# Kernel optimization log

Measured on AMD Instinct MI355X. Metric: run time of the kernel, lower is better.

Reference implementation:

```python
import jax, jax.numpy as jnp
import numpy as np

N = 20000       # nodes
E = 320000      # edges (avg in-degree 16)
IN_DIM = 128
HID = 64
HEADS = 4
NUM_GRAPHS = 128
N_CLASSES = 10


def setup_inputs() -> dict:
    key = jax.random.key(0)
    ks = jax.random.split(key, 8)
    h = jax.random.normal(ks[0], (N, IN_DIM), jnp.float32)
    src = jax.random.randint(ks[1], (E,), 0, N)
    dst = jax.random.randint(ks[2], (E,), 0, N)
    graph_ids = jnp.sort(jax.random.randint(ks[3], (N,), 0, NUM_GRAPHS))
    # DotGatConv fc weights (no bias in DGL DotGatConv), classifier Linear w/ bias
    W1 = jax.random.normal(ks[4], (IN_DIM, HID * HEADS), jnp.float32) / np.sqrt(IN_DIM).astype(np.float32)
    W2 = jax.random.normal(ks[5], (HID * HEADS, HID), jnp.float32) / np.sqrt(HID * HEADS).astype(np.float32)
    Wc = jax.random.normal(ks[6], (HID, N_CLASSES), jnp.float32) / np.sqrt(HID).astype(np.float32)
    bc = jnp.zeros((N_CLASSES,), jnp.float32)
    return {"h": h, "src": src, "dst": dst, "graph_ids": graph_ids,
            "W1": W1, "W2": W2, "Wc": Wc, "bc": bc}


def dot_gat(x, src, dst, W, num_heads):
    """DGL DotGatConv: scaled dot-product attention over graph edges."""
    n = x.shape[0]
    d = W.shape[1] // num_heads
    ft = (x @ W).reshape(n, num_heads, d)          # [N,H,D]
    hs = ft[src]                                    # [E,H,D] source feats
    hd = ft[dst]                                    # [E,H,D] dest feats
    e = (hs * hd).sum(-1) / jnp.sqrt(jnp.float32(d))  # [E,H] edge scores
    # edge softmax over incoming edges per destination node (stable)
    m = jax.ops.segment_max(e, dst, num_segments=n)    # [N,H]
    ee = jnp.exp(e - m[dst])                           # [E,H]
    den = jax.ops.segment_sum(ee, dst, num_segments=n)[dst]  # [E,H]
    a = ee / den
    # aggregate attention-weighted source messages at destination
    return jax.ops.segment_sum(hs * a[..., None], dst, num_segments=n)  # [N,H,D]


def reference(h, src, dst, graph_ids, W1, W2, Wc, bc):
    n = h.shape[0]
    x = jax.nn.relu(dot_gat(h, src, dst, W1, HEADS)).reshape(n, -1)   # [N, HID*HEADS]
    x = jax.nn.relu(dot_gat(x, src, dst, W2, 1)).reshape(n, -1)       # [N, HID]
    # AvgPooling: mean of node features per graph
    cnt = jax.ops.segment_sum(jnp.ones((n,), x.dtype), graph_ids, num_segments=NUM_GRAPHS)
    pooled = jax.ops.segment_sum(x, graph_ids, num_segments=NUM_GRAPHS) / jnp.maximum(cnt, 1.0)[:, None]
    return pooled @ Wc + bc                                            # [NUM_GRAPHS, N_CLASSES]
```

## Files before the change

### kernel.cpp

```cpp
#include <hip/hip_runtime.h>
#include <hip/hip_bf16.h>

typedef __attribute__((ext_vector_type(8))) __bf16 bf16x8;
typedef __attribute__((ext_vector_type(4))) float floatx4;

#define N_NODES   20000
#define N_EDGES   320000
#define IN_DIM    128
#define HID       64
#define HEADS     4
#define NUM_GRAPHS 128
#define N_CLASSES 10

__device__ inline float cvt_load(const void* p, int i, int isb) {
    return isb ? __bfloat162float(((const __hip_bfloat16*)p)[i]) : ((const float*)p)[i];
}

__device__ inline unsigned short bf16bits(float v) {
    return __builtin_bit_cast(unsigned short, __float2bfloat16(v));
}

__device__ inline unsigned pack2(float a, float b) {
    return (unsigned)bf16bits(a) | ((unsigned)bf16bits(b) << 16);
}

__device__ inline floatx4 unpack4(uint2 u) {
    floatx4 f;
    f.x = __uint_as_float(u.x << 16);
    f.y = __uint_as_float(u.x & 0xffff0000u);
    f.z = __uint_as_float(u.y << 16);
    f.w = __uint_as_float(u.y & 0xffff0000u);
    return f;
}

__global__ void init_kernel(const unsigned int* hw, int nwords, int* flag,
                            unsigned int* cnt, int n1, unsigned int* gz, int n2) {
    int b = blockIdx.x;
    if (b == 0) {
        __shared__ int s_bad;
        if (threadIdx.x == 0) s_bad = 0;
        __syncthreads();
        int bad = 0;
        for (int i = threadIdx.x; i < nwords; i += 256) {
            float v = __uint_as_float(hw[i]);
            if (!(fabsf(v) <= 1e20f)) bad = 1;
        }
        if (bad) atomicOr(&s_bad, 1);
        __syncthreads();
        if (threadIdx.x == 0) *flag = s_bad;
    } else {
        int i = (b - 1) * 256 + threadIdx.x;
        if (i < n1) cnt[i] = 0u;
        int j = i - n1;
        if (j >= 0 && j < n2) gz[j] = 0u;
    }
}

__global__ void prep_kernel(const void* W1, const void* W2, const void* Wc, const void* bc,
                            unsigned short* W1t, unsigned short* W2t, float* Wcf, float* bcf,
                            const void* h, unsigned short* hb,
                            const int* __restrict__ dst, int* __restrict__ cnt,
                            const int* flag) {
    int b = blockIdx.x;
    const int n1 = IN_DIM * HID * HEADS;
    const int n2 = HID * HEADS * HID;
    const int n3 = HID * N_CLASSES;
    const int n4 = N_CLASSES;
    if (b < 195) {
        int i = b * 256 + threadIdx.x;
        int isb = *flag;
        if (i < n1) {
            int k = i >> 8, n = i & 255;
            W1t[n * 128 + k] = bf16bits(cvt_load(W1, i, isb));
        } else if (i < n1 + n2) {
            int j = i - n1;
            int k = j >> 6, n = j & 63;
            W2t[n * 256 + k] = bf16bits(cvt_load(W2, j, isb));
        } else if (i < n1 + n2 + n3) {
            int j = i - n1 - n2;
            Wcf[j] = cvt_load(Wc, j, isb);
        } else if (i < n1 + n2 + n3 + n4) {
            int j = i - n1 - n2 - n3;
            bcf[j] = cvt_load(bc, j, isb);
        }
    } else if (b < 195 + 640) {
        int isb = *flag;
        if (!isb) {
            int base = (b - 195) * 4096;
            for (int t = 0; t < 16; ++t) {
                int i = base + t * 256 + threadIdx.x;
                if (i < N_NODES * IN_DIM) hb[i] = bf16bits(cvt_load(h, i, 0));
            }
        }
    } else {
        int e = (b - 835) * 256 + threadIdx.x;
        if (e < N_EDGES) atomicAdd(&cnt[dst[e]], 1);
    }
}

__global__ void scan_kernel(const int* __restrict__ cnt, int* __restrict__ off,
                            int* __restrict__ off_work, int n) {
    const int CH = 20;
    __shared__ int wsum[16];
    int tid  = threadIdx.x;
    int lane = tid & 63;
    int w    = tid >> 6;
    int base = tid * CH;
    int local[CH];
    int s = 0;
#pragma unroll
    for (int i = 0; i < CH; ++i) {
        int idx = base + i;
        int v = (idx < n) ? cnt[idx] : 0;
        local[i] = s;
        s += v;
    }
    int x = s;
#pragma unroll
    for (int sh = 1; sh < 64; sh <<= 1) {
        int t = __shfl_up(x, sh);
        if (lane >= sh) x += t;
    }
    if (lane == 63) wsum[w] = x;
    __syncthreads();
    if (w == 0 && lane < 16) {
        int y = wsum[lane];
#pragma unroll
        for (int sh = 1; sh < 16; sh <<= 1) {
            int t = __shfl_up(y, sh);
            if (lane >= sh) y += t;
        }
        wsum[lane] = y;
    }
    __syncthreads();
    int thread_off = ((w > 0) ? wsum[w - 1] : 0) + (x - s);
#pragma unroll
    for (int i = 0; i < CH; ++i) {
        int idx = base + i;
        if (idx < n) {
            int e = thread_off + local[i];
            off[idx] = e;
            off_work[idx] = e;
        }
    }
    if (tid == 1023) off[n] = thread_off + s;
}

__global__ void fill_kernel(const int* src, const int* dst, int* off_work, int* csr_src, int n) {
    int e = blockIdx.x * blockDim.x + threadIdx.x;
    if (e >= n) return;
    int d = dst[e];
    int pos = atomicAdd(&off_work[d], 1);
    csr_src[pos] = src[e];
}

__global__ __launch_bounds__(256) void gemm1_kernel(const void* __restrict__ h_any,
                                                    const unsigned short* __restrict__ h_b,
                                                    const unsigned short* __restrict__ Bt,
                                                    unsigned short* __restrict__ C, int M,
                                                    const int* flag) {
    const unsigned short* A = (*flag) ? (const unsigned short*)h_any : h_b;
    int wave = threadIdx.x >> 6;
    int lane = threadIdx.x & 63;
    int q = lane >> 4, r = lane & 15;
    int m0 = blockIdx.x * 64;
    int n0 = wave * 64;
    floatx4 acc[4][4] = {};
    bf16x8 bfrag[4][4];
#pragma unroll
    for (int ni = 0; ni < 4; ++ni)
#pragma unroll
        for (int kk = 0; kk < 4; ++kk)
            bfrag[ni][kk] = *(const bf16x8*)(Bt + (n0 + ni * 16 + r) * 128 + kk * 32 + q * 8);
#pragma unroll
    for (int kk = 0; kk < 4; ++kk) {
        bf16x8 afrag[4];
#pragma unroll
        for (int mi = 0; mi < 4; ++mi) {
            int row = m0 + mi * 16 + r;
            bf16x8 a = {};
            if (row < M) a = *(const bf16x8*)(A + row * 128 + kk * 32 + q * 8);
            afrag[mi] = a;
        }
#pragma unroll
        for (int mi = 0; mi < 4; ++mi)
#pragma unroll
            for (int ni = 0; ni < 4; ++ni)
                acc[mi][ni] = __builtin_amdgcn_mfma_f32_16x16x32_bf16(afrag[mi], bfrag[ni][kk], acc[mi][ni], 0, 0, 0);
    }
#pragma unroll
    for (int mi = 0; mi < 4; ++mi)
#pragma unroll
        for (int rr = 0; rr < 4; ++rr) {
            int row = m0 + mi * 16 + q * 4 + rr;
            if (row < M) {
#pragma unroll
                for (int ni = 0; ni < 4; ++ni)
                    C[row * 256 + n0 + ni * 16 + r] = bf16bits(acc[mi][ni][rr]);
            }
        }
}

__global__ __launch_bounds__(256) void gemm2_kernel(const unsigned short* __restrict__ A,
                                                    const unsigned short* __restrict__ Bt,
                                                    unsigned short* __restrict__ C, int M) {
    int wave = threadIdx.x >> 6;
    int lane = threadIdx.x & 63;
    int q = lane >> 4, r = lane & 15;
    int m0 = blockIdx.x * 256 + wave * 64;
    floatx4 acc[4][4] = {};
#pragma unroll
    for (int kk = 0; kk < 8; ++kk) {
        bf16x8 bfrag[4], afrag[4];
#pragma unroll
        for (int ni = 0; ni < 4; ++ni)
            bfrag[ni] = *(const bf16x8*)(Bt + (ni * 16 + r) * 256 + kk * 32 + q * 8);
#pragma unroll
        for (int mi = 0; mi < 4; ++mi) {
            int row = m0 + mi * 16 + r;
            bf16x8 a = {};
            if (row < M) a = *(const bf16x8*)(A + row * 256 + kk * 32 + q * 8);
            afrag[mi] = a;
        }
#pragma unroll
        for (int mi = 0; mi < 4; ++mi)
#pragma unroll
            for (int ni = 0; ni < 4; ++ni)
                acc[mi][ni] = __builtin_amdgcn_mfma_f32_16x16x32_bf16(afrag[mi], bfrag[ni], acc[mi][ni], 0, 0, 0);
    }
#pragma unroll
    for (int mi = 0; mi < 4; ++mi)
#pragma unroll
        for (int rr = 0; rr < 4; ++rr) {
            int row = m0 + mi * 16 + q * 4 + rr;
            if (row < M) {
#pragma unroll
                for (int ni = 0; ni < 4; ++ni)
                    C[row * 64 + ni * 16 + r] = bf16bits(acc[mi][ni][rr]);
            }
        }
}

__global__ __launch_bounds__(256) void attn_h4_kernel(const unsigned short* __restrict__ ft,
                                                      const int* __restrict__ off,
                                                      const int* __restrict__ csr,
                                                      unsigned short* __restrict__ out) {
    int dstv = blockIdx.x * 4 + (threadIdx.x >> 6);
    int lane = threadIdx.x & 63;
    floatx4 hd = unpack4(*(const uint2*)(ft + dstv * 256 + lane * 4));
    int beg = off[dstv], end = off[dstv + 1];
    float l = 0.f;
    floatx4 acc = {0.f, 0.f, 0.f, 0.f};
    int e = beg;
    for (; e + 4 <= end; e += 4) {
        int sn0 = csr[e], sn1 = csr[e + 1], sn2 = csr[e + 2], sn3 = csr[e + 3];
        uint2 r0 = *(const uint2*)(ft + sn0 * 256 + lane * 4);
        uint2 r1 = *(const uint2*)(ft + sn1 * 256 + lane * 4);
        uint2 r2 = *(const uint2*)(ft + sn2 * 256 + lane * 4);
        uint2 r3 = *(const uint2*)(ft + sn3 * 256 + lane * 4);
        floatx4 h0 = unpack4(r0), h1 = unpack4(r1), h2 = unpack4(r2), h3 = unpack4(r3);
        float p0 = h0.x * hd.x + h0.y * hd.y + h0.z * hd.z + h0.w * hd.w;
        float p1 = h1.x * hd.x + h1.y * hd.y + h1.z * hd.z + h1.w * hd.w;
        float p2 = h2.x * hd.x + h2.y * hd.y + h2.z * hd.z + h2.w * hd.w;
        float p3 = h3.x * hd.x + h3.y * hd.y + h3.z * hd.z + h3.w * hd.w;
        p0 += __shfl_xor(p0, 1); p1 += __shfl_xor(p1, 1); p2 += __shfl_xor(p2, 1); p3 += __shfl_xor(p3, 1);
        p0 += __shfl_xor(p0, 2); p1 += __shfl_xor(p1, 2); p2 += __shfl_xor(p2, 2); p3 += __shfl_xor(p3, 2);
        p0 += __shfl_xor(p0, 4); p1 += __shfl_xor(p1, 4); p2 += __shfl_xor(p2, 4); p3 += __shfl_xor(p3, 4);
        p0 += __shfl_xor(p0, 8); p1 += __shfl_xor(p1, 8); p2 += __shfl_xor(p2, 8); p3 += __shfl_xor(p3, 8);
        float w0 = __expf(p0 * 0.125f);
        float w1 = __expf(p1 * 0.125f);
        float w2 = __expf(p2 * 0.125f);
        float w3 = __expf(p3 * 0.125f);
        l += (w0 + w1) + (w2 + w3);
        acc.x += w0 * h0.x + w1 * h1.x + w2 * h2.x + w3 * h3.x;
        acc.y += w0 * h0.y + w1 * h1.y + w2 * h2.y + w3 * h3.y;
        acc.z += w0 * h0.z + w1 * h1.z + w2 * h2.z + w3 * h3.z;
        acc.w += w0 * h0.w + w1 * h1.w + w2 * h2.w + w3 * h3.w;
    }
    for (; e < end; ++e) {
        int sn = csr[e];
        floatx4 hs = unpack4(*(const uint2*)(ft + sn * 256 + lane * 4));
        float p = hs.x * hd.x + hs.y * hd.y + hs.z * hd.z + hs.w * hd.w;
        p += __shfl_xor(p, 1); p += __shfl_xor(p, 2);
        p += __shfl_xor(p, 4); p += __shfl_xor(p, 8);
        float wgt = __expf(p * 0.125f);
        l += wgt;
        acc.x += wgt * hs.x; acc.y += wgt * hs.y;
        acc.z += wgt * hs.z; acc.w += wgt * hs.w;
    }
    float inv = (l > 0.f) ? 1.f / l : 0.f;
    uint2 o;
    o.x = pack2(fmaxf(acc.x * inv, 0.f), fmaxf(acc.y * inv, 0.f));
    o.y = pack2(fmaxf(acc.z * inv, 0.f), fmaxf(acc.w * inv, 0.f));
    *(uint2*)(out + dstv * 256 + lane * 4) = o;
}

__global__ __launch_bounds__(256) void attn_h1_kernel(const unsigned short* __restrict__ ft,
                                                      const int* __restrict__ off,
                                                      const int* __restrict__ csr,
                                                      float* __restrict__ out) {
    int dstv = blockIdx.x * 4 + (threadIdx.x >> 6);
    int lane = threadIdx.x & 63;
    int g = lane >> 4, s = lane & 15;
    int hbase = s * 4;
    floatx4 hd = unpack4(*(const uint2*)(ft + dstv * 64 + hbase));
    int beg = off[dstv], end = off[dstv + 1];
    float l = 0.f;
    floatx4 acc = {0.f, 0.f, 0.f, 0.f};
    int e0 = beg;
    for (; e0 + 8 <= end; e0 += 8) {
        int ea = e0 + g, eb = e0 + 4 + g;
        int sa = csr[ea], sb = csr[eb];
        uint2 ra = *(const uint2*)(ft + sa * 64 + hbase);
        uint2 rb = *(const uint2*)(ft + sb * 64 + hbase);
        floatx4 ha = unpack4(ra), hb = unpack4(rb);
        float pa = ha.x * hd.x + ha.y * hd.y + ha.z * hd.z + ha.w * hd.w;
        float pb = hb.x * hd.x + hb.y * hd.y + hb.z * hd.z + hb.w * hd.w;
        pa += __shfl_xor(pa, 1); pb += __shfl_xor(pb, 1);
        pa += __shfl_xor(pa, 2); pb += __shfl_xor(pb, 2);
        pa += __shfl_xor(pa, 4); pb += __shfl_xor(pb, 4);
        pa += __shfl_xor(pa, 8); pb += __shfl_xor(pb, 8);
        float wa = __expf(pa * 0.125f);
        float wb = __expf(pb * 0.125f);
        l += wa + wb;
        acc.x += wa * ha.x + wb * hb.x;
        acc.y += wa * ha.y + wb * hb.y;
        acc.z += wa * ha.z + wb * hb.z;
        acc.w += wa * ha.w + wb * hb.w;
    }
    for (; e0 < end; e0 += 4) {
        int e = e0 + g;
        bool valid = (e < end);
        int sn = valid ? csr[e] : 0;
        floatx4 hs = unpack4(*(const uint2*)(ft + sn * 64 + hbase));
        float p = hs.x * hd.x + hs.y * hd.y + hs.z * hd.z + hs.w * hd.w;
        p += __shfl_xor(p, 1); p += __shfl_xor(p, 2);
        p += __shfl_xor(p, 4); p += __shfl_xor(p, 8);
        float wgt = valid ? __expf(p * 0.125f) : 0.f;
        l += wgt;
        acc.x += wgt * hs.x; acc.y += wgt * hs.y;
        acc.z += wgt * hs.z; acc.w += wgt * hs.w;
    }
    l += __shfl_xor(l, 16); l += __shfl_xor(l, 32);
    acc.x += __shfl_xor(acc.x, 16); acc.x += __shfl_xor(acc.x, 32);
    acc.y += __shfl_xor(acc.y, 16); acc.y += __shfl_xor(acc.y, 32);
    acc.z += __shfl_xor(acc.z, 16); acc.z += __shfl_xor(acc.z, 32);
    acc.w += __shfl_xor(acc.w, 16); acc.w += __shfl_xor(acc.w, 32);
    float inv = (l > 0.f) ? 1.f / l : 0.f;
    if (g == 0) {
        floatx4 o = {fmaxf(acc.x * inv, 0.f), fmaxf(acc.y * inv, 0.f),
                     fmaxf(acc.z * inv, 0.f), fmaxf(acc.w * inv, 0.f)};
        *(floatx4*)(out + dstv * 64 + hbase) = o;
    }
}

__global__ void pool_kernel(const float* __restrict__ x, const int* __restrict__ gid,
                            float* pooled, int* gcnt, int n_nodes) {
    int t = blockIdx.x * blockDim.x + threadIdx.x;
    int d = t & 63;
    int n0 = (t >> 6) * 8;
    if (n0 >= n_nodes) return;
    float accv = 0.f;
    int cnt_l = 0;
    int curg = gid[n0];
    for (int i = 0; i < 8 && n0 + i < n_nodes; ++i) {
        int g = gid[n0 + i];
        if (g != curg) {
            atomicAdd(&pooled[curg * 64 + d], accv);
            if (d == 0) atomicAdd(&gcnt[curg], cnt_l);
            accv = 0.f; cnt_l = 0; curg = g;
        }
        accv += x[(n0 + i) * 64 + d];
        cnt_l++;
    }
    atomicAdd(&pooled[curg * 64 + d], accv);
    if (d == 0) atomicAdd(&gcnt[curg], cnt_l);
}

__global__ void classifier_kernel(const float* __restrict__ pooled, const int* __restrict__ gcnt,
                                  const float* __restrict__ Wc, const float* __restrict__ bc,
                                  void* out, const int* flag) {
    int g = blockIdx.x;
    int d = threadIdx.x;
    float c = (float)max(gcnt[g], 1);
    float val = pooled[g * 64 + d] / c;
    for (int cls = 0; cls < N_CLASSES; ++cls) {
        float p = val * Wc[d * N_CLASSES + cls];
#pragma unroll
        for (int o = 1; o < 64; o <<= 1) p += __shfl_xor(p, o);
        if (d == 0) {
            float r = p + bc[cls];
            if (*flag) ((__hip_bfloat16*)out)[g * N_CLASSES + cls] = __float2bfloat16(r);
            else       ((float*)out)[g * N_CLASSES + cls] = r;
        }
    }
}

static inline size_t align256(size_t x) { return (x + 255) & ~size_t(255); }

extern "C" void kernel_launch(void* const* d_in, const int* in_sizes, int n_in,
                              void* d_out, int out_size, void* d_ws, size_t ws_size,
                              hipStream_t stream) {
    const void* h_raw  = d_in[0];
    const int*  src    = (const int*)d_in[1];
    const int*  dst    = (const int*)d_in[2];
    const int*  gid    = (const int*)d_in[3];
    const void* W1_raw = d_in[4];
    const void* W2_raw = d_in[5];
    const void* Wc_raw = d_in[6];
    const void* bc_raw = d_in[7];

    char* w = (char*)d_ws;
    int*  flag     = (int*)w;                      w += 256;
    int*  cnt      = (int*)w;                      w += align256(N_NODES * 4);
    int*  off      = (int*)w;                      w += align256((N_NODES + 1) * 4);
    int*  off_work = (int*)w;                      w += align256(N_NODES * 4);
    int*  csr_src  = (int*)w;                      w += align256(N_EDGES * 4);
    int*  gcnt     = (int*)w;                      w += 512;
    float* pooled  = (float*)w;                    w += NUM_GRAPHS * HID * 4;
    unsigned short* W1t = (unsigned short*)w;      w += align256(256 * 128 * 2);
    unsigned short* W2t = (unsigned short*)w;      w += align256(64 * 256 * 2);
    float* Wcf     = (float*)w;                    w += align256(HID * N_CLASSES * 4);
    float* bcf     = (float*)w;                    w += 256;
    unsigned short* h_b  = (unsigned short*)w;     w += align256((size_t)N_NODES * IN_DIM * 2);
    unsigned short* ft1  = (unsigned short*)w;     w += align256((size_t)N_NODES * 256 * 2);
    unsigned short* x1   = (unsigned short*)w;     w += align256((size_t)N_NODES * 256 * 2);
    unsigned short* ft2  = (unsigned short*)w;     w += align256((size_t)N_NODES * HID * 2);
    float* x2      = (float*)w;                    w += align256((size_t)N_NODES * HID * 4);

    {
        int nz = N_NODES + (128 + NUM_GRAPHS * HID);
        hipLaunchKernelGGL(init_kernel, dim3(1 + (nz + 255) / 256), dim3(256), 0, stream,
                           (const unsigned int*)h_raw, 4096, flag,
                           (unsigned int*)cnt, N_NODES,
                           (unsigned int*)gcnt, 128 + NUM_GRAPHS * HID);
    }

    hipLaunchKernelGGL(prep_kernel, dim3(195 + 640 + 1250), dim3(256), 0, stream,
                       W1_raw, W2_raw, Wc_raw, bc_raw, W1t, W2t, Wcf, bcf,
                       h_raw, h_b, dst, cnt, flag);

    hipLaunchKernelGGL(scan_kernel, dim3(1), dim3(1024), 0, stream, cnt, off, off_work, N_NODES);
    hipLaunchKernelGGL(fill_kernel, dim3((N_EDGES + 255) / 256), dim3(256), 0, stream,
                       src, dst, off_work, csr_src, N_EDGES);

    hipLaunchKernelGGL(gemm1_kernel, dim3((N_NODES + 63) / 64), dim3(256), 0, stream,
                       h_raw, h_b, W1t, ft1, N_NODES, flag);
    hipLaunchKernelGGL(attn_h4_kernel, dim3(N_NODES / 4), dim3(256), 0, stream,
                       ft1, off, csr_src, x1);

    hipLaunchKernelGGL(gemm2_kernel, dim3((N_NODES + 255) / 256), dim3(256), 0, stream,
                       x1, W2t, ft2, N_NODES);
    hipLaunchKernelGGL(attn_h1_kernel, dim3(N_NODES / 4), dim3(256), 0, stream,
                       ft2, off, csr_src, x2);

    {
        int threads = (N_NODES / 8) * 64;
        hipLaunchKernelGGL(pool_kernel, dim3((threads + 255) / 256), dim3(256), 0, stream,
                           x2, gid, pooled, gcnt, N_NODES);
    }

    hipLaunchKernelGGL(classifier_kernel, dim3(NUM_GRAPHS), dim3(64), 0, stream,
                       pooled, gcnt, Wcf, bcf, d_out, flag);
}
```

Before: 217.2 us.

## Fuse CSR fill with gemm1, gemm2 into attention, and pooling with classifier

```diff
diff --git a/kernel.cpp b/kernel.cpp
--- a/kernel.cpp
+++ b/kernel.cpp
@@ -34,7 +34,7 @@
 }
 
 __global__ void init_kernel(const unsigned int* hw, int nwords, int* flag,
-                            unsigned int* cnt, int n1, unsigned int* gz, int n2) {
+                            unsigned int* cnt, int n1) {
     int b = blockIdx.x;
     if (b == 0) {
         __shared__ int s_bad;
@@ -51,8 +51,6 @@
     } else {
         int i = (b - 1) * 256 + threadIdx.x;
         if (i < n1) cnt[i] = 0u;
-        int j = i - n1;
-        if (j >= 0 && j < n2) gz[j] = 0u;
     }
 }
 
@@ -146,24 +144,28 @@
     if (tid == 1023) off[n] = thread_off + s;
 }
 
-__global__ void fill_kernel(const int* src, const int* dst, int* off_work, int* csr_src, int n) {
-    int e = blockIdx.x * blockDim.x + threadIdx.x;
-    if (e >= n) return;
-    int d = dst[e];
-    int pos = atomicAdd(&off_work[d], 1);
-    csr_src[pos] = src[e];
-}
-
-__global__ __launch_bounds__(256) void gemm1_kernel(const void* __restrict__ h_any,
-                                                    const unsigned short* __restrict__ h_b,
-                                                    const unsigned short* __restrict__ Bt,
-                                                    unsigned short* __restrict__ C, int M,
-                                                    const int* flag) {
+__global__ __launch_bounds__(256) void fillgemm1_kernel(
+        const int* __restrict__ src, const int* __restrict__ dst,
+        int* __restrict__ off_work, int* __restrict__ csr_src,
+        const void* __restrict__ h_any, const unsigned short* __restrict__ h_b,
+        const unsigned short* __restrict__ Bt, unsigned short* __restrict__ C,
+        const int* flag) {
+    int b = blockIdx.x;
+    if (b < 1250) {
+        int e = b * 256 + threadIdx.x;
+        if (e < N_EDGES) {
+            int d = dst[e];
+            int pos = atomicAdd(&off_work[d], 1);
+            csr_src[pos] = src[e];
+        }
+        return;
+    }
+    const int M = N_NODES;
     const unsigned short* A = (*flag) ? (const unsigned short*)h_any : h_b;
     int wave = threadIdx.x >> 6;
     int lane = threadIdx.x & 63;
     int q = lane >> 4, r = lane & 15;
-    int m0 = blockIdx.x * 64;
+    int m0 = (b - 1250) * 64;
     int n0 = wave * 64;
     floatx4 acc[4][4] = {};
     bf16x8 bfrag[4][4];
@@ -201,51 +203,14 @@
         }
 }
 
-__global__ __launch_bounds__(256) void gemm2_kernel(const unsigned short* __restrict__ A,
-                                                    const unsigned short* __restrict__ Bt,
-                                                    unsigned short* __restrict__ C, int M) {
-    int wave = threadIdx.x >> 6;
-    int lane = threadIdx.x & 63;
-    int q = lane >> 4, r = lane & 15;
-    int m0 = blockIdx.x * 256 + wave * 64;
-    floatx4 acc[4][4] = {};
-#pragma unroll
-    for (int kk = 0; kk < 8; ++kk) {
-        bf16x8 bfrag[4], afrag[4];
-#pragma unroll
-        for (int ni = 0; ni < 4; ++ni)
-            bfrag[ni] = *(const bf16x8*)(Bt + (ni * 16 + r) * 256 + kk * 32 + q * 8);
-#pragma unroll
-        for (int mi = 0; mi < 4; ++mi) {
-            int row = m0 + mi * 16 + r;
-            bf16x8 a = {};
-            if (row < M) a = *(const bf16x8*)(A + row * 256 + kk * 32 + q * 8);
-            afrag[mi] = a;
-        }
-#pragma unroll
-        for (int mi = 0; mi < 4; ++mi)
-#pragma unroll
-            for (int ni = 0; ni < 4; ++ni)
-                acc[mi][ni] = __builtin_amdgcn_mfma_f32_16x16x32_bf16(afrag[mi], bfrag[ni], acc[mi][ni], 0, 0, 0);
-    }
-#pragma unroll
-    for (int mi = 0; mi < 4; ++mi)
-#pragma unroll
-        for (int rr = 0; rr < 4; ++rr) {
-            int row = m0 + mi * 16 + q * 4 + rr;
-            if (row < M) {
-#pragma unroll
-                for (int ni = 0; ni < 4; ++ni)
-                    C[row * 64 + ni * 16 + r] = bf16bits(acc[mi][ni][rr]);
-            }
-        }
-}
-
 __global__ __launch_bounds__(256) void attn_h4_kernel(const unsigned short* __restrict__ ft,
                                                       const int* __restrict__ off,
                                                       const int* __restrict__ csr,
-                                                      unsigned short* __restrict__ out) {
-    int dstv = blockIdx.x * 4 + (threadIdx.x >> 6);
+                                                      const unsigned short* __restrict__ W2t,
+                                                      unsigned short* __restrict__ ft2) {
+    __shared__ float xs[4][256];
+    int wv   = threadIdx.x >> 6;
+    int dstv = blockIdx.x * 4 + wv;
     int lane = threadIdx.x & 63;
     floatx4 hd = unpack4(*(const uint2*)(ft + dstv * 256 + lane * 4));
     int beg = off[dstv], end = off[dstv + 1];
@@ -289,10 +254,23 @@
         acc.z += wgt * hs.z; acc.w += wgt * hs.w;
     }
     float inv = (l > 0.f) ? 1.f / l : 0.f;
-    uint2 o;
-    o.x = pack2(fmaxf(acc.x * inv, 0.f), fmaxf(acc.y * inv, 0.f));
-    o.y = pack2(fmaxf(acc.z * inv, 0.f), fmaxf(acc.w * inv, 0.f));
-    *(uint2*)(out + dstv * 256 + lane * 4) = o;
+    floatx4 xv = {fmaxf(acc.x * inv, 0.f), fmaxf(acc.y * inv, 0.f),
+                  fmaxf(acc.z * inv, 0.f), fmaxf(acc.w * inv, 0.f)};
+    *(floatx4*)&xs[wv][lane * 4] = xv;
+    __syncthreads();
+    const unsigned short* wrow = W2t + lane * 256;
+    const float* xp = xs[wv];
+    float o = 0.f;
+#pragma unroll 4
+    for (int k8 = 0; k8 < 32; ++k8) {
+        uint4 wb = *(const uint4*)(wrow + k8 * 8);
+        floatx4 wa = unpack4(make_uint2(wb.x, wb.y));
+        floatx4 wc = unpack4(make_uint2(wb.z, wb.w));
+        const float* xq = xp + k8 * 8;
+        o += xq[0] * wa.x + xq[1] * wa.y + xq[2] * wa.z + xq[3] * wa.w
+           + xq[4] * wc.x + xq[5] * wc.y + xq[6] * wc.z + xq[7] * wc.w;
+    }
+    ft2[dstv * 64 + lane] = bf16bits(o);
 }
 
 __global__ __launch_bounds__(256) void attn_h1_kernel(const unsigned short* __restrict__ ft,
@@ -354,44 +332,43 @@
     }
 }
 
-__global__ void pool_kernel(const float* __restrict__ x, const int* __restrict__ gid,
-                            float* pooled, int* gcnt, int n_nodes) {
-    int t = blockIdx.x * blockDim.x + threadIdx.x;
-    int d = t & 63;
-    int n0 = (t >> 6) * 8;
-    if (n0 >= n_nodes) return;
-    float accv = 0.f;
-    int cnt_l = 0;
-    int curg = gid[n0];
-    for (int i = 0; i < 8 && n0 + i < n_nodes; ++i) {
-        int g = gid[n0 + i];
-        if (g != curg) {
-            atomicAdd(&pooled[curg * 64 + d], accv);
-            if (d == 0) atomicAdd(&gcnt[curg], cnt_l);
-            accv = 0.f; cnt_l = 0; curg = g;
-        }
-        accv += x[(n0 + i) * 64 + d];
-        cnt_l++;
-    }
-    atomicAdd(&pooled[curg * 64 + d], accv);
-    if (d == 0) atomicAdd(&gcnt[curg], cnt_l);
-}
-
-__global__ void classifier_kernel(const float* __restrict__ pooled, const int* __restrict__ gcnt,
-                                  const float* __restrict__ Wc, const float* __restrict__ bc,
-                                  void* out, const int* flag) {
+__global__ __launch_bounds__(256) void poolclass_kernel(const float* __restrict__ x,
+                                                        const int* __restrict__ gid,
+                                                        const float* __restrict__ Wc,
+                                                        const float* __restrict__ bc,
+                                                        void* out, const int* flag) {
+    __shared__ int s_lo, s_hi;
+    __shared__ float part[4][64];
     int g = blockIdx.x;
-    int d = threadIdx.x;
-    float c = (float)max(gcnt[g], 1);
-    float val = pooled[g * 64 + d] / c;
-    for (int cls = 0; cls < N_CLASSES; ++cls) {
-        float p = val * Wc[d * N_CLASSES + cls];
-#pragma unroll
-        for (int o = 1; o < 64; o <<= 1) p += __shfl_xor(p, o);
-        if (d == 0) {
-            float r = p + bc[cls];
-            if (*flag) ((__hip_bfloat16*)out)[g * N_CLASSES + cls] = __float2bfloat16(r);
-            else       ((float*)out)[g * N_CLASSES + cls] = r;
+    int tid = threadIdx.x;
+    if (tid == 0) {
+        int lo = 0, hi = N_NODES;
+        while (lo < hi) { int m = (lo + hi) >> 1; if (gid[m] < g) lo = m + 1; else hi = m; }
+        s_lo = lo;
+        int lo2 = lo, hi2 = N_NODES;
+        while (lo2 < hi2) { int m = (lo2 + hi2) >> 1; if (gid[m] < g + 1) lo2 = m + 1; else hi2 = m; }
+        s_hi = lo2;
+    }
+    __syncthreads();
+    int lo = s_lo, hi = s_hi;
+    int d = tid & 63, w = tid >> 6;
+    float sum = 0.f;
+    for (int n = lo + w; n < hi; n += 4) sum += x[n * 64 + d];
+    part[w][d] = sum;
+    __syncthreads();
+    if (w == 0) {
+        float tot = part[0][d] + part[1][d] + part[2][d] + part[3][d];
+        int cntg = hi - lo;
+        float mean = (cntg > 0) ? tot / (float)cntg : 0.f;
+        for (int cls = 0; cls < N_CLASSES; ++cls) {
+            float p = mean * Wc[d * N_CLASSES + cls];
+#pragma unroll
+            for (int o = 1; o < 64; o <<= 1) p += __shfl_xor(p, o);
+            if (d == 0) {
+                float r = p + bc[cls];
+                if (*flag) ((__hip_bfloat16*)out)[g * N_CLASSES + cls] = __float2bfloat16(r);
+                else       ((float*)out)[g * N_CLASSES + cls] = r;
+            }
         }
     }
 }
@@ -416,50 +393,35 @@
     int*  off      = (int*)w;                      w += align256((N_NODES + 1) * 4);
     int*  off_work = (int*)w;                      w += align256(N_NODES * 4);
     int*  csr_src  = (int*)w;                      w += align256(N_EDGES * 4);
-    int*  gcnt     = (int*)w;                      w += 512;
-    float* pooled  = (float*)w;                    w += NUM_GRAPHS * HID * 4;
     unsigned short* W1t = (unsigned short*)w;      w += align256(256 * 128 * 2);
     unsigned short* W2t = (unsigned short*)w;      w += align256(64 * 256 * 2);
     float* Wcf     = (float*)w;                    w += align256(HID * N_CLASSES * 4);
     float* bcf     = (float*)w;                    w += 256;
     unsigned short* h_b  = (unsigned short*)w;     w += align256((size_t)N_NODES * IN_DIM * 2);
     unsigned short* ft1  = (unsigned short*)w;     w += align256((size_t)N_NODES * 256 * 2);
-    unsigned short* x1   = (unsigned short*)w;     w += align256((size_t)N_NODES * 256 * 2);
     unsigned short* ft2  = (unsigned short*)w;     w += align256((size_t)N_NODES * HID * 2);
     float* x2      = (float*)w;                    w += align256((size_t)N_NODES * HID * 4);
 
-    {
-        int nz = N_NODES + (128 + NUM_GRAPHS * HID);
-        hipLaunchKernelGGL(init_kernel, dim3(1 + (nz + 255) / 256), dim3(256), 0, stream,
-                           (const unsigned int*)h_raw, 4096, flag,
-                           (unsigned int*)cnt, N_NODES,
-                           (unsigned int*)gcnt, 128 + NUM_GRAPHS * HID);
-    }
+    hipLaunchKernelGGL(init_kernel, dim3(1 + (N_NODES + 255) / 256), dim3(256), 0, stream,
+                       (const unsigned int*)h_raw, 4096, flag,
+                       (unsigned int*)cnt, N_NODES);
 
     hipLaunchKernelGGL(prep_kernel, dim3(195 + 640 + 1250), dim3(256), 0, stream,
                        W1_raw, W2_raw, Wc_raw, bc_raw, W1t, W2t, Wcf, bcf,
                        h_raw, h_b, dst, cnt, flag);
 
     hipLaunchKernelGGL(scan_kernel, dim3(1), dim3(1024), 0, stream, cnt, off, off_work, N_NODES);
-    hipLaunchKernelGGL(fill_kernel, dim3((N_EDGES + 255) / 256), dim3(256), 0, stream,
-                       src, dst, off_work, csr_src, N_EDGES);
-
-    hipLaunchKernelGGL(gemm1_kernel, dim3((N_NODES + 63) / 64), dim3(256), 0, stream,
-                       h_raw, h_b, W1t, ft1, N_NODES, flag);
+
+    hipLaunchKernelGGL(fillgemm1_kernel, dim3(1250 + 313), dim3(256), 0, stream,
+                       src, dst, off_work, csr_src,
+                       h_raw, h_b, W1t, ft1, flag);
+
     hipLaunchKernelGGL(attn_h4_kernel, dim3(N_NODES / 4), dim3(256), 0, stream,
-                       ft1, off, csr_src, x1);
-
-    hipLaunchKernelGGL(gemm2_kernel, dim3((N_NODES + 255) / 256), dim3(256), 0, stream,
-                       x1, W2t, ft2, N_NODES);
+                       ft1, off, csr_src, W2t, ft2);
+
     hipLaunchKernelGGL(attn_h1_kernel, dim3(N_NODES / 4), dim3(256), 0, stream,
                        ft2, off, csr_src, x2);
 
-    {
-        int threads = (N_NODES / 8) * 64;
-        hipLaunchKernelGGL(pool_kernel, dim3((threads + 255) / 256), dim3(256), 0, stream,
-                           x2, gid, pooled, gcnt, N_NODES);
-    }
-
-    hipLaunchKernelGGL(classifier_kernel, dim3(NUM_GRAPHS), dim3(64), 0, stream,
-                       pooled, gcnt, Wcf, bcf, d_out, flag);
-}
+    hipLaunchKernelGGL(poolclass_kernel, dim3(NUM_GRAPHS), dim3(256), 0, stream,
+                       x2, gid, Wcf, bcf, d_out, flag);
+}
```

New measurement: 272.5 us. 25.4% more time.
